# Kernel tuning notes

Measured on AMD Instinct MI355X. Metric: run time of the kernel, lower is better.

Reference implementation:

```python
import jax, jax.numpy as jnp
import numpy as np

EMBED_DIM = 2048
NUM_HEADS = 16
HEAD_DIM = EMBED_DIM // NUM_HEADS
SCALE = 1.0 / float(np.sqrt(HEAD_DIM))
B, L = 2, 2048


def setup_inputs() -> dict:
    key = jax.random.key(0)
    ks = jax.random.split(key, 8)
    s_in = 1.0 / np.sqrt(EMBED_DIM)
    return {
        "query": jax.random.normal(ks[0], (B, L, EMBED_DIM), dtype=jnp.float32),
        "key": jax.random.normal(ks[1], (B, L, EMBED_DIM), dtype=jnp.float32),
        "value": jax.random.normal(ks[2], (B, L, EMBED_DIM), dtype=jnp.float32),
        # in_proj: Linear(E, 3E) -> weight [3E, E], bias [3E]
        "W_in": jax.random.uniform(ks[3], (3 * EMBED_DIM, EMBED_DIM), jnp.float32, -s_in, s_in),
        "b_in": jax.random.uniform(ks[4], (3 * EMBED_DIM,), jnp.float32, -s_in, s_in),
        # out_proj: Linear(E, E) -> weight [E, E], bias [E]
        "W_out": jax.random.uniform(ks[5], (EMBED_DIM, EMBED_DIM), jnp.float32, -s_in, s_in),
        "b_out": jax.random.uniform(ks[6], (EMBED_DIM,), jnp.float32, -s_in, s_in),
    }


def reference(query, key, value, W_in, b_in, W_out, b_out):
    # NOTE: the torch module ignores `key`/`value`; QKV all come from `query`.
    b, t, e = query.shape
    qkv = jnp.einsum("ble,fe->blf", query, W_in) + b_in  # [B, L, 3E]
    q, k, v = jnp.split(qkv, 3, axis=-1)
    # [B, H, L, D]
    q = q.reshape(b, t, NUM_HEADS, HEAD_DIM).transpose(0, 2, 1, 3)
    k = k.reshape(b, -1, NUM_HEADS, HEAD_DIM).transpose(0, 2, 1, 3)
    v = v.reshape(b, -1, NUM_HEADS, HEAD_DIM).transpose(0, 2, 1, 3)
    scores = jnp.einsum("bhqd,bhkd->bhqk", q, k) * SCALE  # [B, H, L, L]
    attn = jax.nn.softmax(scores, axis=-1)
    # torch code zeros attn if any NaN appears (can't happen with no masks);
    # replicate the guard harmlessly:
    attn = jnp.where(jnp.any(jnp.isnan(attn)), jnp.zeros_like(attn), attn)
    ctx = jnp.einsum("bhqk,bhkd->bhqd", attn, v)  # [B, H, L, D]
    ctx = ctx.transpose(0, 2, 1, 3).reshape(b, t, e)  # [B, L, E]
    out = jnp.einsum("ble,fe->blf", ctx, W_out) + b_out
    attn_avg = attn.mean(axis=1)  # [B, L, L]
    return (out, attn_avg)
```

## Files before the change

### kernel.cpp

```cpp
#include <hip/hip_runtime.h>
#include <hip/hip_bf16.h>
#include <stdint.h>
#include <stddef.h>

constexpr int BATCH = 2;
constexpr int SEQ   = 2048;
constexpr int EMBD  = 2048;
constexpr int NHEAD = 16;
constexpr int HDIM  = 128;
constexpr float QSCALE = 0.08838834764831845f * 1.4426950408889634f;

typedef short bf16x8 __attribute__((ext_vector_type(8)));
typedef float f32x4  __attribute__((ext_vector_type(4)));

__device__ __forceinline__ short f2bfs(float f) {
  union { __hip_bfloat16 h; short s; } u;
  u.h = __float2bfloat16(f);
  return u.s;
}

__device__ __forceinline__ void gload_lds16(const void* g, void* l) {
  __builtin_amdgcn_global_load_lds(
      (const __attribute__((address_space(1))) unsigned int*)g,
      (__attribute__((address_space(3))) unsigned int*)l, 16, 0, 0);
}

__device__ __forceinline__ int vperm(int k) {
  return (k & ~31) | (k & 3) | (((k >> 4) & 1) << 2) | (((k >> 2) & 3) << 3);
}

__global__ void cvt_bf16_3(const float* __restrict__ s0, unsigned short* __restrict__ d0, int n0,
                           const float* __restrict__ s1, unsigned short* __restrict__ d1, int n1,
                           const float* __restrict__ s2, unsigned short* __restrict__ d2, int n2) {
  int i = (blockIdx.x * blockDim.x + threadIdx.x) * 8;
  const int stride = gridDim.x * blockDim.x * 8;
  const int t01 = n0 + n1, tot = n0 + n1 + n2;
  for (; i < tot; i += stride) {
    const float* s; unsigned short* d; int off;
    if (i < n0)      { s = s0; d = d0; off = i; }
    else if (i < t01){ s = s1; d = d1; off = i - n0; }
    else             { s = s2; d = d2; off = i - t01; }
    float4 a = *(const float4*)(s + off);
    float4 b = *(const float4*)(s + off + 4);
    union { unsigned short u[8]; int4 v; } r;
    r.u[0] = (unsigned short)f2bfs(a.x); r.u[1] = (unsigned short)f2bfs(a.y);
    r.u[2] = (unsigned short)f2bfs(a.z); r.u[3] = (unsigned short)f2bfs(a.w);
    r.u[4] = (unsigned short)f2bfs(b.x); r.u[5] = (unsigned short)f2bfs(b.y);
    r.u[6] = (unsigned short)f2bfs(b.z); r.u[7] = (unsigned short)f2bfs(b.w);
    *(int4*)(d + off) = r.v;
  }
}

struct EpiQKV {
  const float* bias;
  unsigned short* qs; unsigned short* ks; unsigned short* vti;
  __device__ void operator()(int row, int col, float v) const {
    float val = v + bias[col];
    const int which = col >> 11;
    const int h = (col >> 7) & 15;
    const int d = col & 127;
    const int b = row >> 11, l = row & (SEQ - 1);
    if (which == 0) {
      qs[(((unsigned)(b * NHEAD + h) * SEQ) + l) * HDIM + d] = (unsigned short)f2bfs(val * QSCALE);
    } else if (which == 1) {
      ks[(((unsigned)(b * NHEAD + h) * SEQ) + l) * HDIM + d] = (unsigned short)f2bfs(val);
    } else {
      vti[(((unsigned)(b * NHEAD + h) * HDIM) + d) * SEQ + vperm(l)] = (unsigned short)f2bfs(val);
    }
  }
};

struct EpiOut {
  const float* bias;
  float* out;
  __device__ void operator()(int row, int col, float v) const {
    out[(size_t)row * EMBD + col] = v + bias[col];
  }
};

template <class Epi>
__device__ void gemm_body(unsigned short* ldsbuf,
                          const unsigned short* __restrict__ A,
                          const unsigned short* __restrict__ B,
                          int K, int m0, int n0, Epi epi) {
  const int tid = threadIdx.x;
  const int w = tid >> 6, lane = tid & 63;
  const int g = lane >> 4, lr = lane & 15;
  const int wm = w >> 1, wn = w & 1;
  const int srow = lane >> 2, sslot = lane & 3;

  f32x4 acc[4][4] = {};

  auto stage = [&](int buf, int t) {
    const int k0 = t * 32;
    unsigned short* slot = ldsbuf + buf * 8192;
#pragma unroll
    for (int c2 = 0; c2 < 2; ++c2) {
      const int chunk = 2 * w + c2;
      const int row = chunk * 16 + srow;
      const int kel = k0 + ((sslot ^ ((row >> 1) & 3)) << 3);
      gload_lds16(A + (size_t)(m0 + row) * K + kel, &slot[chunk * 512]);
      gload_lds16(B + (size_t)(n0 + row) * K + kel, &slot[4096 + chunk * 512]);
    }
  };

  const int nt = K >> 5;
  int cur = 0;
  stage(0, 0);
  asm volatile("s_waitcnt vmcnt(0)" ::: "memory");
  __syncthreads();

  for (int t = 0; t < nt; ++t) {
    if (t + 1 < nt) stage(cur ^ 1, t + 1);
    const unsigned short* slot = ldsbuf + cur * 8192;
    bf16x8 af[4], bq[4];
#pragma unroll
    for (int fr = 0; fr < 4; ++fr) {
      const int r = wm * 64 + fr * 16 + lr;
      af[fr] = *(const bf16x8*)&slot[r * 32 + ((g ^ ((r >> 1) & 3)) << 3)];
      const int rn = wn * 64 + fr * 16 + lr;
      bq[fr] = *(const bf16x8*)&slot[4096 + rn * 32 + ((g ^ ((rn >> 1) & 3)) << 3)];
    }
#pragma unroll
    for (int i = 0; i < 4; ++i)
#pragma unroll
      for (int j = 0; j < 4; ++j)
        acc[i][j] = __builtin_amdgcn_mfma_f32_16x16x32_bf16(af[i], bq[j], acc[i][j], 0, 0, 0);
    asm volatile("s_waitcnt vmcnt(0)" ::: "memory");
    __syncthreads();
    cur ^= 1;
  }

#pragma unroll
  for (int i = 0; i < 4; ++i)
#pragma unroll
    for (int j = 0; j < 4; ++j) {
      const int row = m0 + wm * 64 + i * 16 + g * 4;
      const int col = n0 + wn * 64 + j * 16 + lr;
#pragma unroll
      for (int jr = 0; jr < 4; ++jr) epi(row + jr, col, acc[i][j][jr]);
    }
}

__global__ __launch_bounds__(256, 2) void gemm_qkv(
    const unsigned short* __restrict__ A, const unsigned short* __restrict__ B,
    int K, EpiQKV epi) {
  __shared__ __align__(16) unsigned short lds[2][8192];
  gemm_body(&lds[0][0], A, B, K, blockIdx.y * 128, blockIdx.x * 128, epi);
}

__device__ void attn_avg_body(unsigned short* lds,
                              const unsigned short* __restrict__ qs,
                              const unsigned short* __restrict__ ks,
                              const float* __restrict__ c_s,
                              float* __restrict__ out, int blk) {
  const int tid = threadIdx.x, w = tid >> 6, lane = tid & 63;
  const int g = lane >> 4, lr = lane & 15;
  const int wm = w >> 1, wn = w & 1;
  const int k0 = (blk & 15) * 128, q0 = ((blk >> 4) & 15) * 128, b = blk >> 8;
  const int srow = lane >> 2, sslot = lane & 3;

  constexpr int NC = NHEAD * 4;

  auto stage = [&](int c) {
    const size_t bh = ((size_t)(b * NHEAD + (c >> 2))) * SEQ * HDIM + (c & 3) * 32;
    unsigned short* slot = lds + (c % 3) * 8192;
#pragma unroll
    for (int c2 = 0; c2 < 2; ++c2) {
      const int chunk = 2 * w + c2;
      const int row = chunk * 16 + srow;
      const int kel = (sslot ^ ((row >> 1) & 3)) << 3;
      gload_lds16(qs + bh + (size_t)(q0 + row) * HDIM + kel, &slot[chunk * 512]);
      gload_lds16(ks + bh + (size_t)(k0 + row) * HDIM + kel, &slot[4096 + chunk * 512]);
    }
  };

  f32x4 acc[4][4] = {};

  stage(0); stage(1);
  asm volatile("s_waitcnt vmcnt(4)" ::: "memory");
  asm volatile("s_barrier" ::: "memory");

  for (int hc = 0; hc < NHEAD; ++hc) {
    f32x4 st[4][4] = {};
#pragma unroll
    for (int dq = 0; dq < 4; ++dq) {
      const int c = hc * 4 + dq;
      if (c + 2 < NC) stage(c + 2);
      const unsigned short* slot = lds + (c % 3) * 8192;
      bf16x8 af[4], bq[4];
#pragma unroll
      for (int fr = 0; fr < 4; ++fr) {
        const int rq = wm * 64 + fr * 16 + lr;
        af[fr] = *(const bf16x8*)&slot[rq * 32 + ((g ^ ((rq >> 1) & 3)) << 3)];
        const int rk = wn * 64 + fr * 16 + lr;
        bq[fr] = *(const bf16x8*)&slot[4096 + rk * 32 + ((g ^ ((rk >> 1) & 3)) << 3)];
      }
#pragma unroll
      for (int i = 0; i < 4; ++i)
#pragma unroll
        for (int j = 0; j < 4; ++j)
          st[i][j] = __builtin_amdgcn_mfma_f32_16x16x32_bf16(af[i], bq[j], st[i][j], 0, 0, 0);
      if (c + 2 < NC) {
        asm volatile("s_waitcnt vmcnt(4)" ::: "memory");
        asm volatile("s_barrier" ::: "memory");
      } else if (c + 1 < NC) {
        asm volatile("s_waitcnt vmcnt(0)" ::: "memory");
        asm volatile("s_barrier" ::: "memory");
      }
    }
    const int chq = (b * NHEAD + hc) * SEQ + q0 + wm * 64 + g * 4;
#pragma unroll
    for (int i = 0; i < 4; ++i) {
      const f32x4 cq = *(const f32x4*)&c_s[chq + i * 16];
#pragma unroll
      for (int j = 0; j < 4; ++j)
#pragma unroll
        for (int jr = 0; jr < 4; ++jr)
          acc[i][j][jr] += __builtin_exp2f(st[i][j][jr] - cq[jr]);
    }
  }

#pragma unroll
  for (int i = 0; i < 4; ++i)
#pragma unroll
    for (int jr = 0; jr < 4; ++jr) {
      const size_t rowoff = (size_t)(b * SEQ + q0 + wm * 64 + i * 16 + g * 4 + jr) * SEQ;
#pragma unroll
      for (int j = 0; j < 4; ++j)
        out[rowoff + k0 + wn * 64 + j * 16 + lr] = acc[i][j][jr];
    }
}

__global__ __launch_bounds__(256, 2) void tail_fused(
    const unsigned short* __restrict__ ctx, const unsigned short* __restrict__ wo,
    const float* __restrict__ b_out, float* __restrict__ out,
    const unsigned short* __restrict__ qs, const unsigned short* __restrict__ ks,
    const float* __restrict__ c_s, float* __restrict__ attn_avg) {
  __shared__ __align__(16) unsigned short lds[3 * 8192];
  const int id = blockIdx.x;
  if (id < 512) {
    gemm_body(lds, ctx, wo, EMBD, (id >> 4) * 128, (id & 15) * 128, EpiOut{b_out, out});
  } else {
    attn_avg_body(lds, qs, ks, c_s, attn_avg, id - 512);
  }
}

__global__ __launch_bounds__(512, 4) void flash_fwd(
    const unsigned short* __restrict__ qs, const unsigned short* __restrict__ ks,
    const unsigned short* __restrict__ vti, unsigned short* __restrict__ ctx,
    float* __restrict__ c_s) {
  __shared__ __align__(16) unsigned short smem[32768];
  const int tid = threadIdx.x, w = tid >> 6, lane = tid & 63;
  const int g = lane >> 4, lr = lane & 15;
  const int blk = ((int)blockIdx.x & 7) * ((int)gridDim.x >> 3) + ((int)blockIdx.x >> 3);
  const int qt = blk & 15, h = (blk >> 4) & 15, b = blk >> 8;
  const int q0 = qt * 128;
  const size_t bh = ((size_t)(b * NHEAD + h)) * SEQ * HDIM;

  const int qrow = q0 + w * 16 + lr;
  bf16x8 qf[4];
#pragma unroll
  for (int kk = 0; kk < 4; ++kk)
    qf[kk] = *(const bf16x8*)(qs + bh + (size_t)qrow * HDIM + kk * 32 + g * 8);

  float m_run = -1e30f, l_run = 0.f;
  f32x4 o[8] = {};

  auto stage = [&](int buf, int t) {
    unsigned short* kt = smem + buf * 16384;
    unsigned short* vt = kt + 8192;
    const int key0 = t * 64;
#pragma unroll
    for (int c = 0; c < 2; ++c) {
      const int chunk = w * 2 + c;
      const int key = chunk * 4 + (lane >> 4);
      const int slot = lane & 15;
      gload_lds16(ks + bh + (size_t)(key0 + key) * HDIM + ((slot ^ (key & 7)) * 8),
                  &kt[chunk * 512]);
    }
#pragma unroll
    for (int c = 0; c < 2; ++c) {
      const int chunk = w * 2 + c;
      const int d = chunk * 8 + (lane >> 3);
      const int slot = lane & 7;
      gload_lds16(vti + bh + (size_t)d * SEQ + key0 + ((slot ^ (d & 7)) * 8),
                  &vt[chunk * 512]);
    }
  };

  stage(0, 0);
  asm volatile("s_waitcnt vmcnt(0)" ::: "memory");
  __syncthreads();
  int cur = 0;

  for (int t = 0; t < 32; ++t) {
    if (t + 1 < 32) stage(cur ^ 1, t + 1);
    const unsigned short* kt = smem + cur * 16384;
    const unsigned short* vt = kt + 8192;

    f32x4 st[4] = {};
    __builtin_amdgcn_s_setprio(1);
#pragma unroll
    for (int kk = 0; kk < 4; ++kk)
#pragma unroll
      for (int fc = 0; fc < 4; ++fc) {
        const int key = fc * 16 + lr;
        bf16x8 kf = *(const bf16x8*)&kt[key * 128 + (((kk * 4 + g) ^ (key & 7)) << 3)];
        st[fc] = __builtin_amdgcn_mfma_f32_16x16x32_bf16(kf, qf[kk], st[fc], 0, 0, 0);
      }
    __builtin_amdgcn_s_setprio(0);

    float tmax = st[0][0];
#pragma unroll
    for (int fc = 0; fc < 4; ++fc)
#pragma unroll
      for (int j = 0; j < 4; ++j) tmax = fmaxf(tmax, st[fc][j]);
    tmax = fmaxf(tmax, __shfl_xor(tmax, 16));
    tmax = fmaxf(tmax, __shfl_xor(tmax, 32));
    if (!__all(tmax <= m_run + 8.f)) {
      const float m_new = fmaxf(m_run, tmax);
      const float corr = __builtin_exp2f(m_run - m_new);
      l_run *= corr;
#pragma unroll
      for (int fd = 0; fd < 8; ++fd)
#pragma unroll
        for (int j = 0; j < 4; ++j) o[fd][j] *= corr;
      m_run = m_new;
    }
    float pt[4][4];
    float tsum = 0.f;
#pragma unroll
    for (int fc = 0; fc < 4; ++fc)
#pragma unroll
      for (int j = 0; j < 4; ++j) {
        const float e = __builtin_exp2f(st[fc][j] - m_run);
        pt[fc][j] = e; tsum += e;
      }
    tsum += __shfl_xor(tsum, 16);
    tsum += __shfl_xor(tsum, 32);
    l_run += tsum;

    bf16x8 pb[2];
#pragma unroll
    for (int c = 0; c < 2; ++c)
#pragma unroll
      for (int j = 0; j < 4; ++j) {
        pb[c][j]     = f2bfs(pt[2 * c][j]);
        pb[c][4 + j] = f2bfs(pt[2 * c + 1][j]);
      }

    __builtin_amdgcn_s_setprio(1);
#pragma unroll
    for (int fd = 0; fd < 8; ++fd) {
      const int d = fd * 16 + lr;
#pragma unroll
      for (int c = 0; c < 2; ++c) {
        bf16x8 vf = *(const bf16x8*)&vt[d * 64 + (((c * 4 + g) ^ (d & 7)) << 3)];
        o[fd] = __builtin_amdgcn_mfma_f32_16x16x32_bf16(vf, pb[c], o[fd], 0, 0, 0);
      }
    }
    __builtin_amdgcn_s_setprio(0);

    asm volatile("s_waitcnt vmcnt(0)" ::: "memory");
    __syncthreads();
    cur ^= 1;
  }

  const float inv_l = 1.0f / l_run;
  unsigned short* trp = smem + w * 2176;
#pragma unroll
  for (int fd = 0; fd < 8; ++fd)
#pragma unroll
    for (int jp = 0; jp < 2; ++jp) {
      const int d = fd * 16 + 4 * g + 2 * jp;
      unsigned valu = (unsigned)(unsigned short)f2bfs(o[fd][2 * jp] * inv_l) |
                      ((unsigned)(unsigned short)f2bfs(o[fd][2 * jp + 1] * inv_l) << 16);
      *(unsigned*)((char*)trp + lr * 272 + d * 2) = valu;
    }
  __syncthreads();
#pragma unroll
  for (int r4 = 0; r4 < 4; ++r4) {
    const int row = r4 * 4 + g;
    bf16x8 valv = *(const bf16x8*)((char*)trp + row * 272 + lr * 16);
    *(bf16x8*)(ctx + (size_t)(b * SEQ + q0 + w * 16 + row) * EMBD + h * HDIM + lr * 8) = valv;
  }
  if (g == 0) {
    const int ridx = (b * NHEAD + h) * SEQ + q0 + w * 16 + lr;
    c_s[ridx] = m_run + __log2f(l_run) + 4.0f;
  }
}

extern "C" void kernel_launch(void* const* d_in, const int* in_sizes, int n_in,
                              void* d_out, int out_size, void* d_ws, size_t ws_size,
                              hipStream_t stream) {
  const float* query = (const float*)d_in[0];
  const float* W_in  = (const float*)d_in[3];
  const float* b_in  = (const float*)d_in[4];
  const float* W_out = (const float*)d_in[5];
  const float* b_out = (const float*)d_in[6];

  float* out      = (float*)d_out;
  float* attn_avg = out + (size_t)BATCH * SEQ * EMBD;

  char* ws = (char*)d_ws;
  auto take = [&](size_t bytes) { char* p = ws; ws += bytes; return p; };
  const size_t szBLE = (size_t)BATCH * SEQ * EMBD * 2;
  unsigned short* qbf = (unsigned short*)take(szBLE);
  unsigned short* wi  = (unsigned short*)take((size_t)3 * EMBD * EMBD * 2);
  unsigned short* wo  = (unsigned short*)take((size_t)EMBD * EMBD * 2);
  unsigned short* qsb = (unsigned short*)take(szBLE);
  unsigned short* ksb = (unsigned short*)take(szBLE);
  unsigned short* vti = (unsigned short*)take(szBLE);
  unsigned short* ctx = (unsigned short*)take(szBLE);
  float* c_s = (float*)take((size_t)BATCH * NHEAD * SEQ * 4);

  cvt_bf16_3<<<2048, 256, 0, stream>>>(query, qbf, BATCH * SEQ * EMBD,
                                       W_in, wi, 3 * EMBD * EMBD,
                                       W_out, wo, EMBD * EMBD);

  gemm_qkv<<<dim3(48, 32), 256, 0, stream>>>(qbf, wi, EMBD,
                                             EpiQKV{b_in, qsb, ksb, vti});
  flash_fwd<<<BATCH * NHEAD * (SEQ / 128), 512, 0, stream>>>(qsb, ksb, vti, ctx, c_s);
  tail_fused<<<1024, 256, 0, stream>>>(ctx, wo, b_out, out, qsb, ksb, c_s, attn_avg);
}
```

Measured before the change: 376.3 us.

## Replace QKV GEMM with 256x256-tile 8-wave pipelined kernel

Swaps the 128x128 QKV projection GEMM for a new 256x256 tile kernel with 512 threads, K-step 64, XOR-swizzled LDS and quarter-tile staging interleaved with MFMA phases under s_setprio. The goal is higher operand reuse per LDS load and better overlap of global-to-LDS loads with matrix math in the largest GEMM. The cost is 128KB of LDS per block and a grid of only 384 blocks, which can limit occupancy and leave the tail of the grid unbalanced across CUs.

```diff
diff --git a/kernel.cpp b/kernel.cpp
--- a/kernel.cpp
+++ b/kernel.cpp
@@ -78,6 +78,125 @@
   }
 };
 
+__global__ __launch_bounds__(512, 2) void gemm_qkv8(
+    const unsigned short* __restrict__ A, const unsigned short* __restrict__ B,
+    EpiQKV epi) {
+  __shared__ __align__(16) unsigned short lds[2][32768];
+  const int tid = threadIdx.x, w = tid >> 6, lane = tid & 63;
+  const int g = lane >> 4, lr = lane & 15;
+  const int wm = w >> 2, wn = w & 3;
+  const int m0 = ((int)blockIdx.x / 24) * 256;
+  const int n0 = ((int)blockIdx.x % 24) * 256;
+  constexpr int K = 2048;
+  constexpr int nt = K / 64;
+
+  const int srow = tid >> 3, sslot = tid & 7;
+
+  auto stageH = [&](int t, int sel, int hh) {
+    const unsigned short* src = sel ? B : A;
+    const int base0 = sel ? n0 : m0;
+    const int kel = t * 64 + ((sslot ^ (srow & 7)) << 3);
+#pragma unroll
+    for (int l = 0; l < 2; ++l)
+      gload_lds16(src + (size_t)(base0 + hh * 128 + l * 64 + srow) * K + kel,
+                  &lds[t & 1][sel * 16384 + hh * 8192 + (l * 512 + tid) * 8]);
+  };
+  auto rdA = [&](int buf, int Mh, int kk, int fr) -> bf16x8 {
+    const int r = Mh * 128 + wm * 64 + fr * 16 + lr;
+    return *(const bf16x8*)&lds[buf][r * 64 + (((kk * 4 + g) ^ (r & 7)) << 3)];
+  };
+  auto rdB = [&](int buf, int Nh, int kk, int fb) -> bf16x8 {
+    const int r = Nh * 128 + wn * 32 + fb * 16 + lr;
+    return *(const bf16x8*)&lds[buf][16384 + r * 64 + (((kk * 4 + g) ^ (r & 7)) << 3)];
+  };
+
+  f32x4 acc[8][4] = {};
+  bf16x8 a[4][2], bl[2][2], bh[2][2];
+
+  stageH(0, 0, 0); stageH(0, 0, 1); stageH(0, 1, 0); stageH(0, 1, 1);
+  stageH(1, 0, 0); stageH(1, 1, 0); stageH(1, 1, 1);
+  asm volatile("s_waitcnt vmcnt(6)" ::: "memory");
+  __builtin_amdgcn_s_barrier();
+
+  for (int t = 0; t < nt; ++t) {
+    const int buf = t & 1;
+#pragma unroll
+    for (int fr = 0; fr < 4; ++fr) { a[fr][0] = rdA(buf, 0, 0, fr); a[fr][1] = rdA(buf, 0, 1, fr); }
+#pragma unroll
+    for (int fb = 0; fb < 2; ++fb) { bl[fb][0] = rdB(buf, 0, 0, fb); bl[fb][1] = rdB(buf, 0, 1, fb); }
+    if (t + 1 < nt) stageH(t + 1, 0, 1);
+    __builtin_amdgcn_s_barrier();
+    asm volatile("s_waitcnt lgkmcnt(0)" ::: "memory");
+    __builtin_amdgcn_s_setprio(1);
+#pragma unroll
+    for (int fr = 0; fr < 4; ++fr)
+#pragma unroll
+      for (int fb = 0; fb < 2; ++fb)
+#pragma unroll
+        for (int kk = 0; kk < 2; ++kk)
+          acc[fr][fb] = __builtin_amdgcn_mfma_f32_16x16x32_bf16(a[fr][kk], bl[fb][kk], acc[fr][fb], 0, 0, 0);
+    __builtin_amdgcn_s_setprio(0);
+    __builtin_amdgcn_s_barrier();
+#pragma unroll
+    for (int fb = 0; fb < 2; ++fb) { bh[fb][0] = rdB(buf, 1, 0, fb); bh[fb][1] = rdB(buf, 1, 1, fb); }
+    if (t + 2 < nt) stageH(t + 2, 0, 0);
+    __builtin_amdgcn_s_barrier();
+    asm volatile("s_waitcnt lgkmcnt(0)" ::: "memory");
+    __builtin_amdgcn_s_setprio(1);
+#pragma unroll
+    for (int fr = 0; fr < 4; ++fr)
+#pragma unroll
+      for (int fb = 0; fb < 2; ++fb)
+#pragma unroll
+        for (int kk = 0; kk < 2; ++kk)
+          acc[fr][2 + fb] = __builtin_amdgcn_mfma_f32_16x16x32_bf16(a[fr][kk], bh[fb][kk], acc[fr][2 + fb], 0, 0, 0);
+    __builtin_amdgcn_s_setprio(0);
+    __builtin_amdgcn_s_barrier();
+#pragma unroll
+    for (int fr = 0; fr < 4; ++fr) { a[fr][0] = rdA(buf, 1, 0, fr); a[fr][1] = rdA(buf, 1, 1, fr); }
+    if (t + 2 < nt) stageH(t + 2, 1, 0);
+    __builtin_amdgcn_s_barrier();
+    asm volatile("s_waitcnt lgkmcnt(0)" ::: "memory");
+    __builtin_amdgcn_s_setprio(1);
+#pragma unroll
+    for (int fr = 0; fr < 4; ++fr)
+#pragma unroll
+      for (int fb = 0; fb < 2; ++fb)
+#pragma unroll
+        for (int kk = 0; kk < 2; ++kk)
+          acc[4 + fr][2 + fb] = __builtin_amdgcn_mfma_f32_16x16x32_bf16(a[fr][kk], bh[fb][kk], acc[4 + fr][2 + fb], 0, 0, 0);
+    __builtin_amdgcn_s_setprio(0);
+    __builtin_amdgcn_s_barrier();
+    if (t + 2 < nt) stageH(t + 2, 1, 1);
+    __builtin_amdgcn_s_barrier();
+    __builtin_amdgcn_s_setprio(1);
+#pragma unroll
+    for (int fr = 0; fr < 4; ++fr)
+#pragma unroll
+      for (int fb = 0; fb < 2; ++fb)
+#pragma unroll
+        for (int kk = 0; kk < 2; ++kk)
+          acc[4 + fr][fb] = __builtin_amdgcn_mfma_f32_16x16x32_bf16(a[fr][kk], bl[fb][kk], acc[4 + fr][fb], 0, 0, 0);
+    __builtin_amdgcn_s_setprio(0);
+    if (t + 2 < nt) {
+      asm volatile("s_waitcnt vmcnt(6)" ::: "memory");
+    } else if (t + 1 < nt) {
+      asm volatile("s_waitcnt vmcnt(0)" ::: "memory");
+    }
+    __builtin_amdgcn_s_barrier();
+  }
+
+#pragma unroll
+  for (int mf = 0; mf < 8; ++mf)
+#pragma unroll
+    for (int nf = 0; nf < 4; ++nf) {
+      const int row = m0 + (mf >> 2) * 128 + wm * 64 + (mf & 3) * 16 + g * 4;
+      const int col = n0 + (nf >> 1) * 128 + wn * 32 + (nf & 1) * 16 + lr;
+#pragma unroll
+      for (int jr = 0; jr < 4; ++jr) epi(row + jr, col, acc[mf][nf][jr]);
+    }
+}
+
 template <class Epi>
 __device__ void gemm_body(unsigned short* ldsbuf,
                           const unsigned short* __restrict__ A,
@@ -140,13 +259,6 @@
 #pragma unroll
       for (int jr = 0; jr < 4; ++jr) epi(row + jr, col, acc[i][j][jr]);
     }
-}
-
-__global__ __launch_bounds__(256, 2) void gemm_qkv(
-    const unsigned short* __restrict__ A, const unsigned short* __restrict__ B,
-    int K, EpiQKV epi) {
-  __shared__ __align__(16) unsigned short lds[2][8192];
-  gemm_body(&lds[0][0], A, B, K, blockIdx.y * 128, blockIdx.x * 128, epi);
 }
 
 __device__ void attn_avg_body(unsigned short* lds,
@@ -419,8 +531,7 @@
                                        W_in, wi, 3 * EMBD * EMBD,
                                        W_out, wo, EMBD * EMBD);
 
-  gemm_qkv<<<dim3(48, 32), 256, 0, stream>>>(qbf, wi, EMBD,
-                                             EpiQKV{b_in, qsb, ksb, vti});
+  gemm_qkv8<<<16 * 24, 512, 0, stream>>>(qbf, wi, EpiQKV{b_in, qsb, ksb, vti});
   flash_fwd<<<BATCH * NHEAD * (SEQ / 128), 512, 0, stream>>>(qsb, ksb, vti, ctx, c_s);
   tail_fused<<<1024, 256, 0, stream>>>(ctx, wo, b_out, out, qsb, ksb, c_s, attn_avg);
 }
```

Measured after the change: 367.4 us (median of 2 runs). 2.4% less time.
